# Kernel tuning notes

Hardware: AMD Instinct MI355X
Metric: run time of the kernel (lower is better)

The kernel has to match this reference:

```python
import jax, jax.numpy as jnp
import numpy as np

NUM_HEADS = 16
HEAD_DIM = 64
WINDOW = 512  # attention_window; band half-width = WINDOW // 2
MAX_TIME = 10000.0  # rotary default max timescale


def apply_rotary(x):
    """Rotary encoding as in pos_encs_lib.apply_rotary_encoding.

    x: [b, t, h, d]. Pairs (x[2i], x[2i+1]) are rotated by angle pos * inv_freq,
    with inv_freq repeated per pair (interleaved layout).
    """
    d = x.shape[-1]
    freq_seq = jnp.arange(d // 2, dtype=jnp.float32) / (d // 2)
    inv_freq = jnp.repeat(MAX_TIME ** -freq_seq, 2)  # [d]
    pos = jnp.arange(x.shape[1], dtype=jnp.float32)
    t = pos[None, :, None, None] * inv_freq[None, None, None, :]  # [1,t,1,d]
    xp = x.reshape(*x.shape[:-1], d // 2, 2)
    x_rot = jnp.stack([-xp[..., 1], xp[..., 0]], axis=-1).reshape(x.shape)
    return x * jnp.cos(t).astype(x.dtype) + x_rot * jnp.sin(t).astype(x.dtype)


def setup_inputs() -> dict:
    key = jax.random.key(0)
    ks = jax.random.split(key, 6)
    B, T, E = 4, 2048, 1024
    H = NUM_HEADS * HEAD_DIM
    return {
        "inputs_q": jax.random.normal(ks[0], (B, T, E), jnp.float32),
        "inputs_kv": jax.random.normal(ks[1], (B, T, E), jnp.float32),
        "Wq": jax.random.normal(ks[2], (E, H), jnp.float32) * 0.02,
        "Wk": jax.random.normal(ks[3], (E, H), jnp.float32) * 0.02,
        "Wv": jax.random.normal(ks[4], (E, H), jnp.float32) * 0.02,
        "Wo": jax.random.normal(ks[5], (H, E), jnp.float32) * 0.02,
    }


def reference(inputs_q, inputs_kv, Wq, Wk, Wv, Wo):
    b, T, E = inputs_q.shape
    q = (inputs_q @ Wq).reshape(b, T, NUM_HEADS, HEAD_DIM)
    k = (inputs_kv @ Wk).reshape(b, T, NUM_HEADS, HEAD_DIM)
    v = (inputs_kv @ Wv).reshape(b, T, NUM_HEADS, HEAD_DIM)
    q = apply_rotary(q)
    k = apply_rotary(k)
    # [b, h, t, T] attention logits, scaled by 1/sqrt(head_dim)
    att = jnp.einsum('bthd,bThd->bhtT', q, k) * (1.0 / np.sqrt(HEAD_DIM))
    # sliding-window band mask: |i - j| <= WINDOW // 2 (matches k-diagonal sum)
    idx = jnp.arange(T)
    band = jnp.abs(idx[:, None] - idx[None, :]) <= (WINDOW // 2)
    att = jnp.where(band, att, jnp.finfo(jnp.float32).min)
    p = jax.nn.softmax(att, axis=-1)
    out = jnp.einsum('bhtT,bThd->bthd', p, v).reshape(b, T, NUM_HEADS * HEAD_DIM)
    return out @ Wo
```

## Files before the change

kernel.cpp:

```cpp
#include <hip/hip_runtime.h>
#include <hip/hip_bf16.h>


typedef __attribute__((ext_vector_type(8))) short s8v;
typedef __attribute__((ext_vector_type(4))) float f4v;

#define MFMA_BF16 __builtin_amdgcn_mfma_f32_16x16x32_bf16

#define ASYNC_CP16(g, l)                                             \
  __builtin_amdgcn_global_load_lds(                                  \
      (const __attribute__((address_space(1))) void*)(g),            \
      (__attribute__((address_space(3))) void*)(l), 16, 0, 0)

#define SWZ(row, g) ((row) * 64 + ((((g) ^ ((row) & 7))) * 8))

__device__ __forceinline__ unsigned short f2bf(float f) {
  union { float f; unsigned int u; } v; v.f = f;
  unsigned int r = (v.u + 0x7fffu + ((v.u >> 16) & 1u)) >> 16;
  return (unsigned short)r;
}

__device__ __forceinline__ unsigned int pack_bf16(float a, float b) {
  union { __hip_bfloat162 h; unsigned int u; } cv;
  cv.h = __float22bfloat162_rn(make_float2(a, b));
  return cv.u;
}

__global__ __launch_bounds__(256) void cvt2_kernel(
    const float* __restrict__ s0, const float* __restrict__ s1,
    unsigned short* __restrict__ d0, unsigned short* __restrict__ d1) {
  int g = blockIdx.x;
  const float* src = (g < 8192) ? s0 : s1;
  unsigned short* dst = (g < 8192) ? d0 : d1;
  int i = ((g & 8191) * 256 + threadIdx.x) * 4;
  float4 v = *(const float4*)(src + i);
  ushort4 o;
  o.x = f2bf(v.x); o.y = f2bf(v.y); o.z = f2bf(v.z); o.w = f2bf(v.w);
  *(ushort4*)(dst + i) = o;
}

__global__ __launch_bounds__(256) void wtrans_kernel(
    const float* __restrict__ W0, const float* __restrict__ W1,
    const float* __restrict__ W2, const float* __restrict__ W3,
    unsigned short* __restrict__ D0, unsigned short* __restrict__ D1,
    unsigned short* __restrict__ D2, unsigned short* __restrict__ D3) {
  const float* W = blockIdx.z == 0 ? W0 : blockIdx.z == 1 ? W1 : blockIdx.z == 2 ? W2 : W3;
  unsigned short* D = blockIdx.z == 0 ? D0 : blockIdx.z == 1 ? D1 : blockIdx.z == 2 ? D2 : D3;
  __shared__ float tile[32][33];
  int n0 = blockIdx.x * 32, k0 = blockIdx.y * 32;
  int tx = threadIdx.x & 31, ty = threadIdx.x >> 5;
#pragma unroll
  for (int r = 0; r < 32; r += 8)
    tile[ty + r][tx] = W[(size_t)(k0 + ty + r) * 1024 + n0 + tx];
  __syncthreads();
#pragma unroll
  for (int r = 0; r < 32; r += 8)
    D[(size_t)(n0 + ty + r) * 1024 + k0 + tx] = f2bf(tile[tx][ty + r]);
}

__global__ __launch_bounds__(256) void proj_gemm(
    const unsigned short* __restrict__ XqBf, const unsigned short* __restrict__ XkvBf,
    const unsigned short* __restrict__ Wtq, const unsigned short* __restrict__ Wtk,
    const unsigned short* __restrict__ Wtv,
    unsigned short* __restrict__ Qb, unsigned short* __restrict__ Kb,
    unsigned short* __restrict__ Vt) {
  const int K = 1024;
  int z = blockIdx.z;
  const unsigned short* A  = (z == 0) ? XqBf : XkvBf;
  const unsigned short* Bt = (z == 0) ? Wtq : (z == 1) ? Wtk : Wtv;

  __shared__ __align__(16) unsigned short sA[128 * 64];
  __shared__ __align__(16) unsigned short sB[128 * 64];

  int tid = threadIdx.x;
  int lane = tid & 63, wave = tid >> 6;
  int quad = lane >> 4, l16 = lane & 15;
  int wm = wave & 1, wn = wave >> 1;
  int m_blk = blockIdx.x * 128, n_blk = blockIdx.y * 128;

  f4v acc[4][4] = {};
  int srow = tid >> 3, sg = (tid & 7) ^ (srow & 7);
  const unsigned short* gA = A + (size_t)(m_blk + srow) * K + sg * 8;
  const unsigned short* gB = Bt + (size_t)(n_blk + srow) * K + sg * 8;

  for (int k0 = 0; k0 < K; k0 += 64) {
#pragma unroll
    for (int i = 0; i < 4; ++i) {
      ASYNC_CP16(gA + (size_t)i * 32 * K + k0, &sA[i * 2048 + tid * 8]);
      ASYNC_CP16(gB + (size_t)i * 32 * K + k0, &sB[i * 2048 + tid * 8]);
    }
    __syncthreads();
#pragma unroll
    for (int ks = 0; ks < 64; ks += 32) {
      s8v af[4], bf[4];
#pragma unroll
      for (int mt = 0; mt < 4; ++mt)
        af[mt] = *(const s8v*)&sA[SWZ(wm * 64 + mt * 16 + l16, quad + (ks >> 3))];
#pragma unroll
      for (int nt = 0; nt < 4; ++nt)
        bf[nt] = *(const s8v*)&sB[SWZ(wn * 64 + nt * 16 + l16, quad + (ks >> 3))];
#pragma unroll
      for (int mt = 0; mt < 4; ++mt)
#pragma unroll
        for (int nt = 0; nt < 4; ++nt)
          acc[mt][nt] = MFMA_BF16(af[mt], bf[nt], acc[mt][nt], 0, 0, 0);
    }
    __syncthreads();
  }

  if (z < 2) {
    unsigned short* Cb = (z == 0) ? Qb : Kb;
    float post = (z == 0) ? 0.125f : 1.0f;
#pragma unroll
    for (int mt = 0; mt < 4; ++mt)
#pragma unroll
      for (int nt = 0; nt < 4; ++nt)
#pragma unroll
        for (int r = 0; r < 4; ++r) {
          int row = m_blk + wm * 64 + mt * 16 + quad * 4 + r;
          int col = n_blk + wn * 64 + nt * 16 + l16;
          float v = acc[mt][nt][r];
          float other = __shfl_xor(v, 1);
          int dh = col & 63;
          int tpos = row & 2047;
          float fi = (float)(dh >> 1) * (1.0f / 32.0f);
          float invf = __expf(-9.210340371976184f * fi);
          float ang = (float)tpos * invf;
          float s, c;
          __sincosf(ang, &s, &c);
          v = (dh & 1) ? (v * c + other * s) : (v * c - other * s);
          Cb[(size_t)row * 1024 + col] = f2bf(v * post);
        }
  } else {
#pragma unroll
    for (int mt = 0; mt < 4; ++mt)
#pragma unroll
      for (int nt = 0; nt < 4; ++nt) {
        int row0 = m_blk + wm * 64 + mt * 16 + quad * 4;
        int col = n_blk + wn * 64 + nt * 16 + l16;
        int bb = row0 >> 11, t = row0 & 2047;
        int hh = col >> 6, dh = col & 63;
        ushort4 pk;
        pk.x = f2bf(acc[mt][nt][0]);
        pk.y = f2bf(acc[mt][nt][1]);
        pk.z = f2bf(acc[mt][nt][2]);
        pk.w = f2bf(acc[mt][nt][3]);
        *(ushort4*)&Vt[(((size_t)bb * 16 + hh) * 64 + dh) * 2048 + t] = pk;
      }
  }
}

__global__ __launch_bounds__(256, 4) void attn_kernel(
    const unsigned short* __restrict__ Qb, const unsigned short* __restrict__ Kb,
    const unsigned short* __restrict__ Vt, unsigned short* __restrict__ Ab) {
  const int T = 2048;
  int t0 = blockIdx.x * 128;
  int h = blockIdx.y, b = blockIdx.z;
  int tid = threadIdx.x, lane = tid & 63, wave = tid >> 6;
  int quad = lane >> 4, l16 = lane & 15;

  __shared__ __align__(16) unsigned short sK[64][72];
  __shared__ __align__(16) unsigned short sV[64][72];
  __shared__ __align__(16) unsigned short sP[4][16][72];

  size_t base = ((size_t)b * T) * 1024 + (size_t)h * 64;
  size_t vbase = ((size_t)b * 16 + h) * 64 * 2048;
  int qlo = t0 + wave * 32;

  s8v bq[2][2];
#pragma unroll
  for (int f = 0; f < 2; ++f) {
    const unsigned short* g = Qb + base + (size_t)(qlo + f * 16 + l16) * 1024;
    bq[f][0] = *(const s8v*)(g + quad * 8);
    bq[f][1] = *(const s8v*)(g + 32 + quad * 8);
  }

  f4v oacc[2][4] = {};
  float mrow[2] = {-1e30f, -1e30f}, lrow[2] = {0.0f, 0.0f};

  int kv_lo = max(0, t0 - 256);
  int kv_hi = min(T, t0 + 128 + 256);
  int ntiles = (kv_hi - kv_lo) >> 6;

  int srow = tid >> 2, sseg = (tid & 3) * 16;
  const unsigned short* gK = Kb + base + (size_t)(kv_lo + srow) * 1024 + sseg;
  const unsigned short* gV = Vt + vbase + (size_t)srow * 2048 + kv_lo + sseg;
  uint4 rk0 = *(const uint4*)gK, rk1 = *(const uint4*)(gK + 8);
  uint4 rv0 = *(const uint4*)gV, rv1 = *(const uint4*)(gV + 8);

  for (int it = 0; it < ntiles; ++it) {
    int kv0 = kv_lo + (it << 6);
    __syncthreads();
    *(uint4*)&sK[srow][sseg] = rk0;
    *(uint4*)&sK[srow][sseg + 8] = rk1;
    *(uint4*)&sV[srow][sseg] = rv0;
    *(uint4*)&sV[srow][sseg + 8] = rv1;
    __syncthreads();
    if (it + 1 < ntiles) {
      const unsigned short* nK = gK + (size_t)(it + 1) * 64 * 1024;
      const unsigned short* nV = gV + (it + 1) * 64;
      rk0 = *(const uint4*)nK; rk1 = *(const uint4*)(nK + 8);
      rv0 = *(const uint4*)nV; rv1 = *(const uint4*)(nV + 8);
    }
    if (kv0 > qlo + 31 + 256 || kv0 + 63 < qlo - 256) continue;

#pragma unroll
    for (int f = 0; f < 2; ++f) {
      int qf = qlo + f * 16;
      int qg = qf + l16;
      f4v sacc[4];
#pragma unroll
      for (int nt = 0; nt < 4; ++nt) {
        s8v ak0 = *(const s8v*)&sK[nt * 16 + l16][quad * 8];
        s8v ak1 = *(const s8v*)&sK[nt * 16 + l16][32 + quad * 8];
        f4v zz = {};
        zz = MFMA_BF16(ak0, bq[f][0], zz, 0, 0, 0);
        sacc[nt] = MFMA_BF16(ak1, bq[f][1], sacc[nt] = zz, 0, 0, 0);
      }
      bool full = (kv0 >= qf - 241) && (kv0 <= qf + 193);
      if (!full) {
#pragma unroll
        for (int nt = 0; nt < 4; ++nt) {
          int kg = kv0 + nt * 16 + quad * 4;
#pragma unroll
          for (int r = 0; r < 4; ++r) {
            int d = qg - (kg + r);
            if (d > 256 || d < -256) sacc[nt][r] = -1e30f;
          }
        }
      }
      float mymax = sacc[0][0];
#pragma unroll
      for (int nt = 0; nt < 4; ++nt)
#pragma unroll
        for (int r = 0; r < 4; ++r) mymax = fmaxf(mymax, sacc[nt][r]);
      mymax = fmaxf(mymax, __shfl_xor(mymax, 16));
      mymax = fmaxf(mymax, __shfl_xor(mymax, 32));

      float mn = fmaxf(mrow[f], mymax);
      float alpha = __expf(mrow[f] - mn);
      mrow[f] = mn;

      float mysum = 0.0f;
#pragma unroll
      for (int nt = 0; nt < 4; ++nt) {
        float e0 = __expf(sacc[nt][0] - mn);
        float e1 = __expf(sacc[nt][1] - mn);
        float e2 = __expf(sacc[nt][2] - mn);
        float e3 = __expf(sacc[nt][3] - mn);
        mysum += (e0 + e1) + (e2 + e3);
        *(uint2*)&sP[wave][l16][nt * 16 + quad * 4] =
            make_uint2(pack_bf16(e0, e1), pack_bf16(e2, e3));
      }
      mysum += __shfl_xor(mysum, 16);
      mysum += __shfl_xor(mysum, 32);
      lrow[f] = lrow[f] * alpha + mysum;

      s8v pb0 = *(const s8v*)&sP[wave][l16][quad * 8];
      s8v pb1 = *(const s8v*)&sP[wave][l16][32 + quad * 8];

#pragma unroll
      for (int dt = 0; dt < 4; ++dt) {
        s8v av0 = *(const s8v*)&sV[dt * 16 + l16][quad * 8];
        s8v av1 = *(const s8v*)&sV[dt * 16 + l16][32 + quad * 8];
        f4v o = oacc[f][dt];
#pragma unroll
        for (int r = 0; r < 4; ++r) o[r] *= alpha;
        o = MFMA_BF16(av0, pb0, o, 0, 0, 0);
        oacc[f][dt] = MFMA_BF16(av1, pb1, o, 0, 0, 0);
      }
    }
  }

#pragma unroll
  for (int f = 0; f < 2; ++f) {
    float inv = 1.0f / lrow[f];
    size_t rowoff = base + (size_t)(qlo + f * 16 + l16) * 1024;
#pragma unroll
    for (int dt = 0; dt < 4; ++dt) {
      float o0 = oacc[f][dt][0] * inv, o1 = oacc[f][dt][1] * inv;
      float o2 = oacc[f][dt][2] * inv, o3 = oacc[f][dt][3] * inv;
      *(uint2*)&Ab[rowoff + dt * 16 + quad * 4] =
          make_uint2(pack_bf16(o0, o1), pack_bf16(o2, o3));
    }
  }
}

__global__ __launch_bounds__(256) void out_gemm(
    const unsigned short* __restrict__ A, const unsigned short* __restrict__ Bt,
    float* __restrict__ C) {
  const int K = 1024;
  __shared__ __align__(16) unsigned short sA[128 * 64];
  __shared__ __align__(16) unsigned short sB[128 * 64];

  int tid = threadIdx.x;
  int lane = tid & 63, wave = tid >> 6;
  int quad = lane >> 4, l16 = lane & 15;
  int wm = wave & 1, wn = wave >> 1;
  int m_blk = blockIdx.x * 128, n_blk = blockIdx.y * 128;

  f4v acc[4][4] = {};
  int srow = tid >> 3, sg = (tid & 7) ^ (srow & 7);
  const unsigned short* gA = A + (size_t)(m_blk + srow) * K + sg * 8;
  const unsigned short* gB = Bt + (size_t)(n_blk + srow) * K + sg * 8;

  for (int k0 = 0; k0 < K; k0 += 64) {
#pragma unroll
    for (int i = 0; i < 4; ++i) {
      ASYNC_CP16(gA + (size_t)i * 32 * K + k0, &sA[i * 2048 + tid * 8]);
      ASYNC_CP16(gB + (size_t)i * 32 * K + k0, &sB[i * 2048 + tid * 8]);
    }
    __syncthreads();
#pragma unroll
    for (int ks = 0; ks < 64; ks += 32) {
      s8v af[4], bf[4];
#pragma unroll
      for (int mt = 0; mt < 4; ++mt)
        af[mt] = *(const s8v*)&sA[SWZ(wm * 64 + mt * 16 + l16, quad + (ks >> 3))];
#pragma unroll
      for (int nt = 0; nt < 4; ++nt)
        bf[nt] = *(const s8v*)&sB[SWZ(wn * 64 + nt * 16 + l16, quad + (ks >> 3))];
#pragma unroll
      for (int mt = 0; mt < 4; ++mt)
#pragma unroll
        for (int nt = 0; nt < 4; ++nt)
          acc[mt][nt] = MFMA_BF16(af[mt], bf[nt], acc[mt][nt], 0, 0, 0);
    }
    __syncthreads();
  }

#pragma unroll
  for (int mt = 0; mt < 4; ++mt)
#pragma unroll
    for (int nt = 0; nt < 4; ++nt)
#pragma unroll
      for (int r = 0; r < 4; ++r) {
        int row = m_blk + wm * 64 + mt * 16 + quad * 4 + r;
        int col = n_blk + wn * 64 + nt * 16 + l16;
        C[(size_t)row * 1024 + col] = acc[mt][nt][r];
      }
}

extern "C" void kernel_launch(void* const* d_in, const int* in_sizes, int n_in,
                              void* d_out, int out_size, void* d_ws, size_t ws_size,
                              hipStream_t stream) {
  const float* Xq  = (const float*)d_in[0];
  const float* Xkv = (const float*)d_in[1];
  const float* Wq  = (const float*)d_in[2];
  const float* Wk  = (const float*)d_in[3];
  const float* Wv  = (const float*)d_in[4];
  const float* Wo  = (const float*)d_in[5];
  float* out = (float*)d_out;

  char* ws = (char*)d_ws;
  const size_t MB = 1ull << 20;
  unsigned short* XqBf  = (unsigned short*)(ws + 0 * MB);
  unsigned short* XkvBf = (unsigned short*)(ws + 16 * MB);
  unsigned short* Wtq   = (unsigned short*)(ws + 32 * MB);
  unsigned short* Wtk   = (unsigned short*)(ws + 34 * MB);
  unsigned short* Wtv   = (unsigned short*)(ws + 36 * MB);
  unsigned short* Wto   = (unsigned short*)(ws + 38 * MB);
  unsigned short* Qb    = (unsigned short*)(ws + 40 * MB);
  unsigned short* Kb    = (unsigned short*)(ws + 56 * MB);
  unsigned short* Vt    = (unsigned short*)(ws + 72 * MB);
  unsigned short* Ab    = XqBf;

  cvt2_kernel<<<16384, 256, 0, stream>>>(Xq, Xkv, XqBf, XkvBf);
  wtrans_kernel<<<dim3(32, 32, 4), 256, 0, stream>>>(Wq, Wk, Wv, Wo, Wtq, Wtk, Wtv, Wto);
  proj_gemm<<<dim3(64, 8, 3), 256, 0, stream>>>(XqBf, XkvBf, Wtq, Wtk, Wtv, Qb, Kb, Vt);
  attn_kernel<<<dim3(16, 16, 4), 256, 0, stream>>>(Qb, Kb, Vt, Ab);
  out_gemm<<<dim3(64, 8), 256, 0, stream>>>(Ab, Wto, out);
}
```

Measured before the change: 259.0 us.

## Merge prep kernels and double attention query tile to 256 rows

Fuses the activation bf16 conversion and weight transpose into one prep kernel launch, removing a kernel launch boundary. The attention kernel now uses 512-thread blocks covering 256 query rows, so each K/V tile staged in shared memory is reused by eight waves instead of four, reducing redundant halo K/V loads across blocks. Each thread now loads one 16-byte chunk per tile instead of two. The trade-off is half as many attention blocks (512 vs 1024) and lower occupancy bound, which may reduce latency hiding.

```diff
diff --git a/kernel.cpp b/kernel.cpp
--- a/kernel.cpp
+++ b/kernel.cpp
@@ -26,36 +26,39 @@
   return cv.u;
 }
 
-__global__ __launch_bounds__(256) void cvt2_kernel(
+__global__ __launch_bounds__(256) void prep_kernel(
     const float* __restrict__ s0, const float* __restrict__ s1,
-    unsigned short* __restrict__ d0, unsigned short* __restrict__ d1) {
-  int g = blockIdx.x;
-  const float* src = (g < 8192) ? s0 : s1;
-  unsigned short* dst = (g < 8192) ? d0 : d1;
-  int i = ((g & 8191) * 256 + threadIdx.x) * 4;
-  float4 v = *(const float4*)(src + i);
-  ushort4 o;
-  o.x = f2bf(v.x); o.y = f2bf(v.y); o.z = f2bf(v.z); o.w = f2bf(v.w);
-  *(ushort4*)(dst + i) = o;
-}
-
-__global__ __launch_bounds__(256) void wtrans_kernel(
+    unsigned short* __restrict__ d0, unsigned short* __restrict__ d1,
     const float* __restrict__ W0, const float* __restrict__ W1,
     const float* __restrict__ W2, const float* __restrict__ W3,
     unsigned short* __restrict__ D0, unsigned short* __restrict__ D1,
     unsigned short* __restrict__ D2, unsigned short* __restrict__ D3) {
-  const float* W = blockIdx.z == 0 ? W0 : blockIdx.z == 1 ? W1 : blockIdx.z == 2 ? W2 : W3;
-  unsigned short* D = blockIdx.z == 0 ? D0 : blockIdx.z == 1 ? D1 : blockIdx.z == 2 ? D2 : D3;
-  __shared__ float tile[32][33];
-  int n0 = blockIdx.x * 32, k0 = blockIdx.y * 32;
-  int tx = threadIdx.x & 31, ty = threadIdx.x >> 5;
-#pragma unroll
-  for (int r = 0; r < 32; r += 8)
-    tile[ty + r][tx] = W[(size_t)(k0 + ty + r) * 1024 + n0 + tx];
-  __syncthreads();
-#pragma unroll
-  for (int r = 0; r < 32; r += 8)
-    D[(size_t)(n0 + ty + r) * 1024 + k0 + tx] = f2bf(tile[tx][ty + r]);
+  int g = blockIdx.x;
+  if (g < 16384) {
+    const float* src = (g < 8192) ? s0 : s1;
+    unsigned short* dst = (g < 8192) ? d0 : d1;
+    int i = ((g & 8191) * 256 + threadIdx.x) * 4;
+    float4 v = *(const float4*)(src + i);
+    ushort4 o;
+    o.x = f2bf(v.x); o.y = f2bf(v.y); o.z = f2bf(v.z); o.w = f2bf(v.w);
+    *(ushort4*)(dst + i) = o;
+  } else {
+    int w = g - 16384;
+    int z = w >> 10;
+    int rem = w & 1023;
+    const float* W = z == 0 ? W0 : z == 1 ? W1 : z == 2 ? W2 : W3;
+    unsigned short* D = z == 0 ? D0 : z == 1 ? D1 : z == 2 ? D2 : D3;
+    __shared__ float tile[32][33];
+    int n0 = (rem & 31) * 32, k0 = (rem >> 5) * 32;
+    int tx = threadIdx.x & 31, ty = threadIdx.x >> 5;
+#pragma unroll
+    for (int r = 0; r < 32; r += 8)
+      tile[ty + r][tx] = W[(size_t)(k0 + ty + r) * 1024 + n0 + tx];
+    __syncthreads();
+#pragma unroll
+    for (int r = 0; r < 32; r += 8)
+      D[(size_t)(n0 + ty + r) * 1024 + k0 + tx] = f2bf(tile[tx][ty + r]);
+  }
 }
 
 __global__ __launch_bounds__(256) void proj_gemm(
@@ -150,18 +153,18 @@
   }
 }
 
-__global__ __launch_bounds__(256, 4) void attn_kernel(
+__global__ __launch_bounds__(512, 2) void attn_kernel(
     const unsigned short* __restrict__ Qb, const unsigned short* __restrict__ Kb,
     const unsigned short* __restrict__ Vt, unsigned short* __restrict__ Ab) {
   const int T = 2048;
-  int t0 = blockIdx.x * 128;
+  int t0 = blockIdx.x * 256;
   int h = blockIdx.y, b = blockIdx.z;
   int tid = threadIdx.x, lane = tid & 63, wave = tid >> 6;
   int quad = lane >> 4, l16 = lane & 15;
 
   __shared__ __align__(16) unsigned short sK[64][72];
   __shared__ __align__(16) unsigned short sV[64][72];
-  __shared__ __align__(16) unsigned short sP[4][16][72];
+  __shared__ __align__(16) unsigned short sP[8][16][72];
 
   size_t base = ((size_t)b * T) * 1024 + (size_t)h * 64;
   size_t vbase = ((size_t)b * 16 + h) * 64 * 2048;
@@ -179,28 +182,24 @@
   float mrow[2] = {-1e30f, -1e30f}, lrow[2] = {0.0f, 0.0f};
 
   int kv_lo = max(0, t0 - 256);
-  int kv_hi = min(T, t0 + 128 + 256);
+  int kv_hi = min(T, t0 + 256 + 256);
   int ntiles = (kv_hi - kv_lo) >> 6;
 
-  int srow = tid >> 2, sseg = (tid & 3) * 16;
+  int srow = tid >> 3, sseg = (tid & 7) * 8;
   const unsigned short* gK = Kb + base + (size_t)(kv_lo + srow) * 1024 + sseg;
   const unsigned short* gV = Vt + vbase + (size_t)srow * 2048 + kv_lo + sseg;
-  uint4 rk0 = *(const uint4*)gK, rk1 = *(const uint4*)(gK + 8);
-  uint4 rv0 = *(const uint4*)gV, rv1 = *(const uint4*)(gV + 8);
+  uint4 rk = *(const uint4*)gK;
+  uint4 rv = *(const uint4*)gV;
 
   for (int it = 0; it < ntiles; ++it) {
     int kv0 = kv_lo + (it << 6);
     __syncthreads();
-    *(uint4*)&sK[srow][sseg] = rk0;
-    *(uint4*)&sK[srow][sseg + 8] = rk1;
-    *(uint4*)&sV[srow][sseg] = rv0;
-    *(uint4*)&sV[srow][sseg + 8] = rv1;
+    *(uint4*)&sK[srow][sseg] = rk;
+    *(uint4*)&sV[srow][sseg] = rv;
     __syncthreads();
     if (it + 1 < ntiles) {
-      const unsigned short* nK = gK + (size_t)(it + 1) * 64 * 1024;
-      const unsigned short* nV = gV + (it + 1) * 64;
-      rk0 = *(const uint4*)nK; rk1 = *(const uint4*)(nK + 8);
-      rv0 = *(const uint4*)nV; rv1 = *(const uint4*)(nV + 8);
+      rk = *(const uint4*)(gK + (size_t)(it + 1) * 64 * 1024);
+      rv = *(const uint4*)(gV + (it + 1) * 64);
     }
     if (kv0 > qlo + 31 + 256 || kv0 + 63 < qlo - 256) continue;
 
@@ -215,7 +214,7 @@
         s8v ak1 = *(const s8v*)&sK[nt * 16 + l16][32 + quad * 8];
         f4v zz = {};
         zz = MFMA_BF16(ak0, bq[f][0], zz, 0, 0, 0);
-        sacc[nt] = MFMA_BF16(ak1, bq[f][1], sacc[nt] = zz, 0, 0, 0);
+        sacc[nt] = MFMA_BF16(ak1, bq[f][1], zz, 0, 0, 0);
       }
       bool full = (kv0 >= qf - 241) && (kv0 <= qf + 193);
       if (!full) {
@@ -365,9 +364,9 @@
   unsigned short* Vt    = (unsigned short*)(ws + 72 * MB);
   unsigned short* Ab    = XqBf;
 
-  cvt2_kernel<<<16384, 256, 0, stream>>>(Xq, Xkv, XqBf, XkvBf);
-  wtrans_kernel<<<dim3(32, 32, 4), 256, 0, stream>>>(Wq, Wk, Wv, Wo, Wtq, Wtk, Wtv, Wto);
+  prep_kernel<<<20480, 256, 0, stream>>>(Xq, Xkv, XqBf, XkvBf,
+                                         Wq, Wk, Wv, Wo, Wtq, Wtk, Wtv, Wto);
   proj_gemm<<<dim3(64, 8, 3), 256, 0, stream>>>(XqBf, XkvBf, Wtq, Wtk, Wtv, Qb, Kb, Vt);
-  attn_kernel<<<dim3(16, 16, 4), 256, 0, stream>>>(Qb, Kb, Vt, Ab);
+  attn_kernel<<<dim3(8, 16, 4), 512, 0, stream>>>(Qb, Kb, Vt, Ab);
   out_gemm<<<dim3(64, 8), 256, 0, stream>>>(Ab, Wto, out);
 }
```

Result: faster. 250.1 us (-3.4%).
